# Optimization experiments

Hardware: AMD Instinct MI355X
Metric: run time of the kernel (lower is better)

The kernel has to match this reference:

```python
import jax, jax.numpy as jnp
import numpy as np

B, SQ, SKV, DIN, DOUT = 8, 2048, 2048, 512, 512

def setup_inputs() -> dict:
    key = jax.random.key(0)
    ks = jax.random.split(key, 8)
    s = 1.0 / np.sqrt(DIN)
    return {
        "query": jax.random.normal(ks[0], (B, SQ, DIN), jnp.float32),
        "key": jax.random.normal(ks[1], (B, SKV, DIN), jnp.float32),
        "value": jax.random.normal(ks[2], (B, SKV, DIN), jnp.float32),
        "offset": jax.random.normal(ks[3], (B, SQ, DIN), jnp.float32),
        "Wq": jax.random.normal(ks[4], (DIN, DOUT), jnp.float32) * s,
        "Wk": jax.random.normal(ks[5], (DIN, DOUT), jnp.float32) * s,
        "Wv": jax.random.normal(ks[6], (DIN, DOUT), jnp.float32) * s,
        "Woff": jax.random.normal(ks[7], (DIN, SKV), jnp.float32) * s,
    }

def reference(query, key, value, offset, Wq, Wk, Wv, Woff):
    # q/k/v projections (nn.Linear, no bias)
    q = jnp.einsum("bqi,io->bqo", query, Wq)   # [B,SQ,DOUT]
    k = jnp.einsum("bki,io->bko", key, Wk)     # [B,SKV,DOUT]
    v = jnp.einsum("bki,io->bko", value, Wv)   # [B,SKV,DOUT]
    scale = 1.0 / jnp.sqrt(jnp.asarray(q.shape[-1], jnp.float32))
    scores = jnp.einsum("bqd,bkd->bqk", q, k) * scale  # [B,SQ,SKV]
    attn = jax.nn.softmax(scores, axis=-1)
    # offset bias is added AFTER softmax (no renormalization), per original
    attn = attn + jnp.einsum("bqi,ik->bqk", offset, Woff)
    return jnp.einsum("bqk,bkd->bqd", attn, v)  # [B,SQ,DOUT]
```

## Files before the change

### kernel.cpp

```cpp
#include <hip/hip_runtime.h>
#include <hip/hip_bf16.h>
#include <stdint.h>

typedef __bf16 bf16;
typedef unsigned char u8;
typedef bf16 bf16x4_t __attribute__((ext_vector_type(4)));
typedef bf16 bf16x8_t __attribute__((ext_vector_type(8)));
typedef float floatx4_t __attribute__((ext_vector_type(4)));

#define NB 8
#define SQ 2048
#define SKV 2048
#define DIN 512
#define DOUT 512

#define SCORE_SCALE 0.0027621358640099513f
#define P_STORE_SCALE 0.0625f
#define P_UNDO_SCALE 16.0f

__device__ __forceinline__ void load_lds16(const void* g, void* l) {
    __builtin_amdgcn_global_load_lds(
        (const __attribute__((address_space(1))) unsigned int*)g,
        (__attribute__((address_space(3))) unsigned int*)l, 16, 0, 0);
}

__device__ __forceinline__ u8 to_fp8(float f) {
    int v = __builtin_amdgcn_cvt_pk_fp8_f32(f, 0.f, 0, false);
    return (u8)(v & 0xff);
}
__device__ __forceinline__ unsigned int pack_fp8x4(float a, float b, float c, float d) {
    int lo = __builtin_amdgcn_cvt_pk_fp8_f32(a, b, 0, false);
    int all = __builtin_amdgcn_cvt_pk_fp8_f32(c, d, lo, true);
    return (unsigned int)all;
}

__device__ __forceinline__ int swz_off(int row, int col) {
    return (col & ~127) | ((((col >> 4) & 7) ^ (row & 7)) << 4) | (col & 15);
}

struct CastArgs {
    const float* src[6];
    void* dst[6];
    int n4[6];
    int mode[6];
};
__global__ void cast_many(CastArgs a) {
    int z = blockIdx.z;
    int i = blockIdx.x * blockDim.x + threadIdx.x;
    if (i >= a.n4[z]) return;
    if (a.mode[z] == 2) {
        ((float4*)a.dst[z])[i] = make_float4(0.f, 0.f, 0.f, 0.f);
        return;
    }
    float4 f = ((const float4*)a.src[z])[i];
    if (a.mode[z] == 1) {
        int row = i >> 7;
        int k0 = (i & 127) * 4;
        u8* d = (u8*)a.dst[z];
        *(unsigned int*)&d[row * 512 + swz_off(row, k0)] = pack_fp8x4(f.x, f.y, f.z, f.w);
    } else {
        bf16x4_t o = { (bf16)f.x, (bf16)f.y, (bf16)f.z, (bf16)f.w };
        ((bf16x4_t*)a.dst[z])[i] = o;
    }
}

struct TWArgs { const float* src[3]; void* dst[3]; };
__global__ void transpose_w(TWArgs a) {
    __shared__ float t[32][33];
    const float* src = a.src[blockIdx.z];
    int tx = threadIdx.x, ty = threadIdx.y;
    int x0 = blockIdx.x * 32, y0 = blockIdx.y * 32;
#pragma unroll
    for (int j = 0; j < 4; ++j)
        t[ty + 8 * j][tx] = src[(y0 + ty + 8 * j) * DIN + x0 + tx];
    __syncthreads();
    if (blockIdx.z <= 1) {
        u8* d8 = (u8*)a.dst[blockIdx.z];
#pragma unroll
        for (int j = 0; j < 4; ++j) {
            int row = x0 + ty + 8 * j, col = y0 + tx;
            d8[row * 512 + swz_off(row, col)] = to_fp8(t[tx][ty + 8 * j] * 4.0f);
        }
    } else {
        bf16* db = (bf16*)a.dst[2];
#pragma unroll
        for (int j = 0; j < 4; ++j)
            db[(x0 + ty + 8 * j) * DIN + y0 + tx] = (bf16)t[tx][ty + 8 * j];
    }
}

__device__ __forceinline__ void gemm_mainloop(
    floatx4_t (&acc)[4][4], const bf16* __restrict__ Ap, const bf16* __restrict__ Bp,
    int lda, int ldb, int K, bf16* As, bf16* Bs, int wave, int lane)
{
    const int wm = (wave & 1) * 64, wn = (wave >> 1) * 64;
    const int lm = lane & 15, quad = lane >> 4;
    const int srow = lane >> 2, scol = (lane & 3) * 8;
    for (int k0 = 0; k0 < K; k0 += 64) {
        __syncthreads();
#pragma unroll
        for (int p = 0; p < 2; ++p) {
#pragma unroll
            for (int t = 0; t < 2; ++t) {
                const int r0 = (wave * 2 + t) * 16;
                load_lds16(Ap + (long long)(r0 + srow) * lda + (k0 + p * 32 + scol),
                           &As[p * 4096 + r0 * 32]);
                load_lds16(Bp + (long long)(r0 + srow) * ldb + (k0 + p * 32 + scol),
                           &Bs[p * 4096 + r0 * 32]);
            }
        }
        __syncthreads();
#pragma unroll
        for (int p = 0; p < 2; ++p) {
            bf16x8_t af[4], bfr[4];
#pragma unroll
            for (int i = 0; i < 4; ++i)
                af[i] = *(const bf16x8_t*)&As[p * 4096 + (wm + i * 16 + lm) * 32 + quad * 8];
#pragma unroll
            for (int i = 0; i < 4; ++i)
                bfr[i] = *(const bf16x8_t*)&Bs[p * 4096 + (wn + i * 16 + lm) * 32 + quad * 8];
#pragma unroll
            for (int i = 0; i < 4; ++i)
#pragma unroll
                for (int j = 0; j < 4; ++j)
                    acc[i][j] = __builtin_amdgcn_mfma_f32_16x16x32_bf16(af[i], bfr[j], acc[i][j], 0, 0, 0);
        }
    }
}

__device__ __forceinline__ void gemm_mainloop_fp8(
    floatx4_t (&acc)[4][4], const u8* __restrict__ Ap, const u8* __restrict__ Bp,
    int lda, int ldb, int K, u8* As, u8* Bs, int wave, int lane)
{
    const int wm = (wave & 1) * 64, wn = (wave >> 1) * 64;
    const int lm = lane & 15, quad = lane >> 4;
    const int srow = lane >> 3, scol = (lane & 7) * 16;
    const int x7 = lm & 7;
    const int inner = (quad & 1) * 8;
    const int gh = quad >> 1;
    for (int k0 = 0; k0 < K; k0 += 128) {
        __syncthreads();
#pragma unroll
        for (int t = 0; t < 4; ++t) {
            const int r0 = (wave * 4 + t) * 8;
            load_lds16(Ap + (long long)(r0 + srow) * lda + k0 + scol, &As[r0 * 128]);
            load_lds16(Bp + (long long)(r0 + srow) * ldb + k0 + scol, &Bs[r0 * 128]);
        }
        __syncthreads();
#pragma unroll
        for (int p = 0; p < 4; ++p) {
            const int gL = p * 2 + gh;
            const int koff = ((gL ^ x7) << 4) + inner;
            long long a[4], b[4];
#pragma unroll
            for (int i = 0; i < 4; ++i)
                a[i] = *(const long long*)&As[(wm + i * 16 + lm) * 128 + koff];
#pragma unroll
            for (int i = 0; i < 4; ++i)
                b[i] = *(const long long*)&Bs[(wn + i * 16 + lm) * 128 + koff];
#pragma unroll
            for (int i = 0; i < 4; ++i)
#pragma unroll
                for (int j = 0; j < 4; ++j)
                    acc[i][j] = __builtin_amdgcn_mfma_f32_16x16x32_fp8_fp8(a[i], b[j], acc[i][j], 0, 0, 0);
        }
    }
}

__global__ __launch_bounds__(256) void proj_gemm(
    const u8* __restrict__ query8, const u8* __restrict__ key8,
    const u8* __restrict__ WqT8, const u8* __restrict__ WkT8,
    u8* __restrict__ Qb8, u8* __restrict__ Kb8,
    const bf16* __restrict__ valueb, const bf16* __restrict__ WvT,
    bf16* __restrict__ VT, u8* __restrict__ VT8)
{
    __shared__ __align__(16) u8 smem[32768];
    const int tid = threadIdx.x;
    const int wave = tid >> 6, lane = tid & 63;
    const int wm = (wave & 1) * 64, wn = (wave >> 1) * 64;
    const int lm = lane & 15, quad = lane >> 4;
    const int id = blockIdx.x;

    floatx4_t acc[4][4];
#pragma unroll
    for (int i = 0; i < 4; ++i)
#pragma unroll
        for (int j = 0; j < 4; ++j) acc[i][j] = 0.0f;

    if (id < 1024) {
        const int xcd = id & 7, t = id >> 3, m = t & 3;
        const int gg = xcd + 8 * (t >> 2);
        const int y = gg & 127, z = gg >> 7;
        const u8* Ap = (z ? key8 : query8) + (long long)y * 128 * DIN;
        const u8* Bp = (z ? WkT8 : WqT8) + (long long)m * 128 * DIN;
        gemm_mainloop_fp8(acc, Ap, Bp, DIN, DIN, DIN, smem, smem + 16384, wave, lane);
        u8* C = z ? Kb8 : Qb8;
#pragma unroll
        for (int i = 0; i < 4; ++i)
#pragma unroll
            for (int j = 0; j < 4; ++j) {
                const int row0 = y * 128 + wm + i * 16 + quad * 4;
                const int col = m * 128 + wn + j * 16 + lm;
#pragma unroll
                for (int r = 0; r < 4; ++r)
                    C[(long long)(row0 + r) * DOUT + swz_off(row0 + r, col)] = to_fp8(acc[i][j][r]);
            }
    } else {
        const int id2 = id - 1024;
        const int z = id2 & 7, r2 = id2 >> 3;
        const int ym = r2 & 3, xn = r2 >> 2;
        const bf16* Ap = WvT + (long long)ym * 128 * DIN;
        const bf16* Bp = valueb + (long long)z * (SKV * DIN) + (long long)xn * 128 * DIN;
        gemm_mainloop(acc, Ap, Bp, DIN, DIN, DIN, (bf16*)smem, (bf16*)(smem + 16384), wave, lane);
        bf16* C = VT + (long long)z * (DOUT * SKV);
        u8* C8 = VT8 + (long long)z * (DOUT * SKV);
#pragma unroll
        for (int i = 0; i < 4; ++i)
#pragma unroll
            for (int j = 0; j < 4; ++j) {
                const int row0 = ym * 128 + wm + i * 16 + quad * 4;
                const int col = xn * 128 + wn + j * 16 + lm;
#pragma unroll
                for (int r = 0; r < 4; ++r) {
                    float v = acc[i][j][r];
                    C[(long long)(row0 + r) * SKV + col] = (bf16)v;
                    C8[(long long)(row0 + r) * SKV + swz_off(row0 + r, col)] = to_fp8(v);
                }
            }
    }
}

__global__ __launch_bounds__(256) void g_gemm(
    const bf16* __restrict__ VT, const bf16* __restrict__ Woffb,
    float* __restrict__ G32a, float* __restrict__ G32b)
{
    __shared__ __align__(16) u8 smem[32768];
    const int tid = threadIdx.x;
    const int wave = tid >> 6, lane = tid & 63;
    const int id = blockIdx.x;
    const int z = id & 7, h = (id >> 3) & 1, x = (id >> 4) & 3, y = (id >> 6) & 3;

    floatx4_t acc[4][4];
#pragma unroll
    for (int i = 0; i < 4; ++i)
#pragma unroll
        for (int j = 0; j < 4; ++j) acc[i][j] = 0.0f;

    const bf16* Ap = VT + (long long)z * (DOUT * SKV) + (long long)y * 128 * SKV + h * 1024;
    const bf16* Bp = Woffb + (long long)x * 128 * SKV + h * 1024;
    gemm_mainloop(acc, Ap, Bp, SKV, SKV, 1024, (bf16*)smem, (bf16*)(smem + 16384), wave, lane);

    const int wm = (wave & 1) * 64, wn = (wave >> 1) * 64;
    const int lm = lane & 15, quad = lane >> 4;
    float* C = (h ? G32b : G32a) + (long long)z * (DOUT * DIN);
#pragma unroll
    for (int i = 0; i < 4; ++i)
#pragma unroll
        for (int j = 0; j < 4; ++j) {
            const int row0 = y * 128 + wm + i * 16 + quad * 4;
            const int col = x * 128 + wn + j * 16 + lm;
#pragma unroll
            for (int r = 0; r < 4; ++r)
                C[(long long)(row0 + r) * DIN + col] = acc[i][j][r];
        }
}

__global__ __launch_bounds__(256) void s_gemm_exp(
    const u8* __restrict__ Qb8, const u8* __restrict__ Kb8,
    u8* __restrict__ expS8, float* __restrict__ l,
    const float* __restrict__ G32a, const float* __restrict__ G32b,
    bf16* __restrict__ Gb)
{
    __shared__ __align__(16) u8 smem[32768];
    const int tid = threadIdx.x;
    const int id = blockIdx.x;
    if (id >= 2048) {
        const int base = (id - 2048) * 256 + tid;
        const float4* A4 = (const float4*)G32a;
        const float4* B4 = (const float4*)G32b;
        bf16x4_t* O4 = (bf16x4_t*)Gb;
#pragma unroll 4
        for (int t = 0; t < 32; ++t) {
            const int idx = base + t * 16384;
            float4 a = A4[idx], b = B4[idx];
            bf16x4_t o = { (bf16)(a.x + b.x), (bf16)(a.y + b.y),
                           (bf16)(a.z + b.z), (bf16)(a.w + b.w) };
            O4[idx] = o;
        }
        return;
    }
    const int wave = tid >> 6, lane = tid & 63;
    const int z = id & 7, x = (id >> 3) & 15, y = (id >> 3) >> 4;

    floatx4_t acc[4][4];
#pragma unroll
    for (int i = 0; i < 4; ++i)
#pragma unroll
        for (int j = 0; j < 4; ++j) acc[i][j] = 0.0f;

    const u8* Ap = Qb8 + ((long long)z * SQ + (long long)y * 128) * DOUT;
    const u8* Bp = Kb8 + ((long long)z * SKV + (long long)x * 128) * DOUT;
    gemm_mainloop_fp8(acc, Ap, Bp, DOUT, DOUT, DOUT, smem, smem + 16384, wave, lane);

    const int wm = (wave & 1) * 64, wn = (wave >> 1) * 64;
    const int lm = lane & 15, quad = lane >> 4;
    u8* C = expS8 + (long long)z * SQ * SKV;
    const long long grow0 = (long long)z * SQ + (long long)y * 128;
#pragma unroll
    for (int i = 0; i < 4; ++i) {
        float rs[4] = {0.f, 0.f, 0.f, 0.f};
#pragma unroll
        for (int j = 0; j < 4; ++j) {
            const int row0 = y * 128 + wm + i * 16 + quad * 4;
            const int col = x * 128 + wn + j * 16 + lm;
#pragma unroll
            for (int r = 0; r < 4; ++r) {
                float e = __expf(acc[i][j][r] * SCORE_SCALE);
                rs[r] += e;
                C[(long long)(row0 + r) * SKV + swz_off(row0 + r, col)] = to_fp8(e * P_STORE_SCALE);
            }
        }
#pragma unroll
        for (int r = 0; r < 4; ++r) {
            float v = rs[r];
            v += __shfl_xor(v, 1, 64);
            v += __shfl_xor(v, 2, 64);
            v += __shfl_xor(v, 4, 64);
            v += __shfl_xor(v, 8, 64);
            if (lm == 0)
                atomicAdd(&l[grow0 + wm + i * 16 + quad * 4 + r], v);
        }
    }
}

__global__ __launch_bounds__(256) void out_gemm(
    const u8* __restrict__ expS8, const u8* __restrict__ VT8,
    const bf16* __restrict__ offb, const bf16* __restrict__ Gb,
    const float* __restrict__ l, float* __restrict__ out)
{
    __shared__ __align__(16) u8 smem[32768];
    const int tid = threadIdx.x;
    const int wave = tid >> 6, lane = tid & 63;
    const int id = blockIdx.x;
    const int z = id & 7, x = (id >> 3) & 3, y = (id >> 3) >> 2;

    floatx4_t acc[4][4];
#pragma unroll
    for (int i = 0; i < 4; ++i)
#pragma unroll
        for (int j = 0; j < 4; ++j) acc[i][j] = 0.0f;

    {
        const u8* Ap = expS8 + (long long)z * SQ * SKV + (long long)y * 128 * SKV;
        const u8* Bp = VT8 + (long long)z * DOUT * SKV + (long long)x * 128 * SKV;
        gemm_mainloop_fp8(acc, Ap, Bp, SKV, SKV, SKV, smem, smem + 16384, wave, lane);
    }

    const int wm = (wave & 1) * 64, wn = (wave >> 1) * 64;
    const int lm = lane & 15, quad = lane >> 4;
    const long long grow0 = (long long)z * SQ + (long long)y * 128;

#pragma unroll
    for (int i = 0; i < 4; ++i)
#pragma unroll
        for (int r = 0; r < 4; ++r) {
            const float inv = P_UNDO_SCALE / l[grow0 + wm + i * 16 + quad * 4 + r];
#pragma unroll
            for (int j = 0; j < 4; ++j) acc[i][j][r] *= inv;
        }

    {
        const bf16* Ap = offb + grow0 * DIN;
        const bf16* Bp = Gb + (long long)z * DOUT * DIN + (long long)x * 128 * DIN;
        gemm_mainloop(acc, Ap, Bp, DIN, DIN, DIN, (bf16*)smem, (bf16*)(smem + 16384), wave, lane);
    }

#pragma unroll
    for (int i = 0; i < 4; ++i)
#pragma unroll
        for (int j = 0; j < 4; ++j) {
            const long long row0 = grow0 + wm + i * 16 + quad * 4;
            const int col = x * 128 + wn + j * 16 + lm;
#pragma unroll
            for (int r = 0; r < 4; ++r)
                out[(row0 + r) * DOUT + col] = acc[i][j][r];
        }
}

extern "C" void kernel_launch(void* const* d_in, const int* in_sizes, int n_in,
                              void* d_out, int out_size, void* d_ws, size_t ws_size,
                              hipStream_t stream) {
    const float* query = (const float*)d_in[0];
    const float* key_ = (const float*)d_in[1];
    const float* value = (const float*)d_in[2];
    const float* offset = (const float*)d_in[3];
    const float* Wq = (const float*)d_in[4];
    const float* Wk = (const float*)d_in[5];
    const float* Wv = (const float*)d_in[6];
    const float* Woff = (const float*)d_in[7];
    float* out = (float*)d_out;

    char* ws = (char*)d_ws;
    const long long NE = (long long)NB * SQ * DIN;
    const long long MB = 1048576;

    u8* query8   = (u8*)(ws + 0 * MB);
    u8* key8     = (u8*)(ws + 8 * MB);
    bf16* valueb = (bf16*)(ws + 16 * MB);
    bf16* offsetb= (bf16*)(ws + 32 * MB);
    u8* Qb8      = (u8*)(ws + 48 * MB);
    u8* Kb8      = (u8*)(ws + 56 * MB);
    bf16* VT     = (bf16*)(ws + 64 * MB);
    u8* VT8      = (u8*)(ws + 80 * MB);
    float* G32a  = (float*)(ws + 88 * MB);
    float* G32b  = (float*)(ws + 96 * MB);
    bf16* Gb     = (bf16*)(ws + 104 * MB);
    u8* WqT8     = (u8*)(ws + 108 * MB);
    u8* WkT8     = (u8*)(ws + 108 * MB + 262144);
    bf16* WvT    = (bf16*)(ws + 108 * MB + 524288);
    bf16* Woffb  = (bf16*)(ws + 109 * MB);
    float* lbuf  = (float*)(ws + 111 * MB);
    u8* expS8    = (u8*)(ws + 112 * MB);

    CastArgs ca;
    ca.src[0] = query;  ca.dst[0] = query8;  ca.n4[0] = (int)(NE / 4); ca.mode[0] = 1;
    ca.src[1] = key_;   ca.dst[1] = key8;    ca.n4[1] = (int)(NE / 4); ca.mode[1] = 1;
    ca.src[2] = value;  ca.dst[2] = valueb;  ca.n4[2] = (int)(NE / 4); ca.mode[2] = 0;
    ca.src[3] = offset; ca.dst[3] = offsetb; ca.n4[3] = (int)(NE / 4); ca.mode[3] = 0;
    ca.src[4] = Woff;   ca.dst[4] = Woffb;   ca.n4[4] = (DIN * SKV) / 4; ca.mode[4] = 0;
    ca.src[5] = nullptr; ca.dst[5] = lbuf;   ca.n4[5] = (NB * SQ) / 4; ca.mode[5] = 2;
    cast_many<<<dim3(8192, 1, 6), 256, 0, stream>>>(ca);

    TWArgs tw;
    tw.src[0] = Wq; tw.src[1] = Wk; tw.src[2] = Wv;
    tw.dst[0] = WqT8; tw.dst[1] = WkT8; tw.dst[2] = WvT;
    transpose_w<<<dim3(16, 16, 3), dim3(32, 8), 0, stream>>>(tw);

    proj_gemm<<<dim3(1536), 256, 0, stream>>>(query8, key8, WqT8, WkT8, Qb8, Kb8,
                                              valueb, WvT, VT, VT8);

    g_gemm<<<dim3(256), 256, 0, stream>>>(VT, Woffb, G32a, G32b);

    s_gemm_exp<<<dim3(2112), 256, 0, stream>>>(Qb8, Kb8, expS8, lbuf, G32a, G32b, Gb);

    out_gemm<<<dim3(512), 256, 0, stream>>>(expS8, VT8, offsetb, Gb, lbuf, out);
}
```

Measured before the change: 333.2 us.

## Double-buffer LDS in bf16 and fp8 GEMM mainloops with halved K-step

Both GEMM mainloops now use two LDS buffers. The next K-slice is prefetched with global_load_lds while MFMAs run on the current one, leaving one barrier per iteration instead of two. The K-step is halved to fit two buffers in the same shared memory. The fp8 swizzle is narrowed from 8 to 4 16-byte groups to match the 64-byte rows. This is meant to hide global-to-LDS latency, at the cost of twice as many loop iterations and barriers per K and a narrower XOR swizzle that may raise LDS bank conflicts.

```diff
diff --git a/kernel.cpp b/kernel.cpp
--- a/kernel.cpp
+++ b/kernel.cpp
@@ -35,7 +35,7 @@
 }
 
 __device__ __forceinline__ int swz_off(int row, int col) {
-    return (col & ~127) | ((((col >> 4) & 7) ^ (row & 7)) << 4) | (col & 15);
+    return (col & ~63) | ((((col >> 4) & 3) ^ (row & 3)) << 4) | (col & 15);
 }
 
 struct CastArgs {
@@ -96,35 +96,37 @@
     const int wm = (wave & 1) * 64, wn = (wave >> 1) * 64;
     const int lm = lane & 15, quad = lane >> 4;
     const int srow = lane >> 2, scol = (lane & 3) * 8;
-    for (int k0 = 0; k0 < K; k0 += 64) {
+
+    auto STAGE = [&](int buf, int k0) {
+#pragma unroll
+        for (int t = 0; t < 2; ++t) {
+            const int r0 = (wave * 2 + t) * 16;
+            load_lds16(Ap + (long long)(r0 + srow) * lda + (k0 + scol),
+                       &As[buf * 4096 + r0 * 32]);
+            load_lds16(Bp + (long long)(r0 + srow) * ldb + (k0 + scol),
+                       &Bs[buf * 4096 + r0 * 32]);
+        }
+    };
+
+    STAGE(0, 0);
+    __syncthreads();
+    int cur = 0;
+    for (int k0 = 0; k0 < K; k0 += 32) {
+        if (k0 + 32 < K) STAGE(cur ^ 1, k0 + 32);
+        bf16x8_t af[4], bfr[4];
+#pragma unroll
+        for (int i = 0; i < 4; ++i)
+            af[i] = *(const bf16x8_t*)&As[cur * 4096 + (wm + i * 16 + lm) * 32 + quad * 8];
+#pragma unroll
+        for (int i = 0; i < 4; ++i)
+            bfr[i] = *(const bf16x8_t*)&Bs[cur * 4096 + (wn + i * 16 + lm) * 32 + quad * 8];
+#pragma unroll
+        for (int i = 0; i < 4; ++i)
+#pragma unroll
+            for (int j = 0; j < 4; ++j)
+                acc[i][j] = __builtin_amdgcn_mfma_f32_16x16x32_bf16(af[i], bfr[j], acc[i][j], 0, 0, 0);
         __syncthreads();
-#pragma unroll
-        for (int p = 0; p < 2; ++p) {
-#pragma unroll
-            for (int t = 0; t < 2; ++t) {
-                const int r0 = (wave * 2 + t) * 16;
-                load_lds16(Ap + (long long)(r0 + srow) * lda + (k0 + p * 32 + scol),
-                           &As[p * 4096 + r0 * 32]);
-                load_lds16(Bp + (long long)(r0 + srow) * ldb + (k0 + p * 32 + scol),
-                           &Bs[p * 4096 + r0 * 32]);
-            }
-        }
-        __syncthreads();
-#pragma unroll
-        for (int p = 0; p < 2; ++p) {
-            bf16x8_t af[4], bfr[4];
-#pragma unroll
-            for (int i = 0; i < 4; ++i)
-                af[i] = *(const bf16x8_t*)&As[p * 4096 + (wm + i * 16 + lm) * 32 + quad * 8];
-#pragma unroll
-            for (int i = 0; i < 4; ++i)
-                bfr[i] = *(const bf16x8_t*)&Bs[p * 4096 + (wn + i * 16 + lm) * 32 + quad * 8];
-#pragma unroll
-            for (int i = 0; i < 4; ++i)
-#pragma unroll
-                for (int j = 0; j < 4; ++j)
-                    acc[i][j] = __builtin_amdgcn_mfma_f32_16x16x32_bf16(af[i], bfr[j], acc[i][j], 0, 0, 0);
-        }
+        cur ^= 1;
     }
 }
 
@@ -134,36 +136,44 @@
 {
     const int wm = (wave & 1) * 64, wn = (wave >> 1) * 64;
     const int lm = lane & 15, quad = lane >> 4;
-    const int srow = lane >> 3, scol = (lane & 7) * 16;
-    const int x7 = lm & 7;
+    const int srow = lane >> 2, scol = (lane & 3) * 16;
+    const int x3 = lm & 3;
     const int inner = (quad & 1) * 8;
     const int gh = quad >> 1;
-    for (int k0 = 0; k0 < K; k0 += 128) {
-        __syncthreads();
-#pragma unroll
-        for (int t = 0; t < 4; ++t) {
-            const int r0 = (wave * 4 + t) * 8;
-            load_lds16(Ap + (long long)(r0 + srow) * lda + k0 + scol, &As[r0 * 128]);
-            load_lds16(Bp + (long long)(r0 + srow) * ldb + k0 + scol, &Bs[r0 * 128]);
-        }
-        __syncthreads();
-#pragma unroll
-        for (int p = 0; p < 4; ++p) {
+
+    auto STAGE = [&](int buf, int k0) {
+#pragma unroll
+        for (int t = 0; t < 2; ++t) {
+            const int r0 = (wave * 2 + t) * 16;
+            load_lds16(Ap + (long long)(r0 + srow) * lda + k0 + scol, &As[buf * 8192 + r0 * 64]);
+            load_lds16(Bp + (long long)(r0 + srow) * ldb + k0 + scol, &Bs[buf * 8192 + r0 * 64]);
+        }
+    };
+
+    STAGE(0, 0);
+    __syncthreads();
+    int cur = 0;
+    for (int k0 = 0; k0 < K; k0 += 64) {
+        if (k0 + 64 < K) STAGE(cur ^ 1, k0 + 64);
+#pragma unroll
+        for (int p = 0; p < 2; ++p) {
             const int gL = p * 2 + gh;
-            const int koff = ((gL ^ x7) << 4) + inner;
+            const int koff = ((gL ^ x3) << 4) + inner;
             long long a[4], b[4];
 #pragma unroll
             for (int i = 0; i < 4; ++i)
-                a[i] = *(const long long*)&As[(wm + i * 16 + lm) * 128 + koff];
+                a[i] = *(const long long*)&As[cur * 8192 + (wm + i * 16 + lm) * 64 + koff];
 #pragma unroll
             for (int i = 0; i < 4; ++i)
-                b[i] = *(const long long*)&Bs[(wn + i * 16 + lm) * 128 + koff];
+                b[i] = *(const long long*)&Bs[cur * 8192 + (wn + i * 16 + lm) * 64 + koff];
 #pragma unroll
             for (int i = 0; i < 4; ++i)
 #pragma unroll
                 for (int j = 0; j < 4; ++j)
                     acc[i][j] = __builtin_amdgcn_mfma_f32_16x16x32_fp8_fp8(a[i], b[j], acc[i][j], 0, 0, 0);
         }
+        __syncthreads();
+        cur ^= 1;
     }
 }
 
```

New measurement: 324.6 us. 2.6% less time.
